# Optimization experiments

Measured on AMD Instinct MI355X. Metric: run time of the kernel, lower is better.

## Reference

```python
import jax, jax.numpy as jnp
import numpy as np

N, C, K2 = 40000, 128, 9  # active voxels, channels, 3x3 kernel taps
HEAD_OUT = {"hm": 3, "center": 2, "center_z": 1, "dim": 3, "rot": 2}
EPS = 1e-5
INIT_BIAS = -2.66


def setup_inputs() -> dict:
    key = jax.random.key(0)
    ks = jax.random.split(key, 16)
    feats = jax.random.normal(ks[0], (N, C), dtype=jnp.float32)
    # precomputed submanifold-conv neighbor indices (one per kernel tap, all valid)
    nbr_idx = jax.random.randint(ks[1], (N, K2), 0, N, dtype=jnp.int32)
    H = len(HEAD_OUT)
    inp = {"feats": feats, "nbr_idx": nbr_idx}
    # stacked 3x3 SubMConv weights for all heads (kaiming-ish scale)
    inp["W1"] = jax.random.normal(ks[2], (H, K2, C, C), dtype=jnp.float32) * (2.0 / (K2 * C)) ** 0.5
    inp["gamma"] = jnp.ones((H, C), jnp.float32)
    inp["beta"] = jnp.zeros((H, C), jnp.float32)
    for i, (name, oc) in enumerate(HEAD_OUT.items()):
        inp[f"w_{name}"] = jax.random.normal(ks[3 + i], (C, oc), dtype=jnp.float32) * (2.0 / C) ** 0.5
        inp[f"b_{name}"] = (jnp.full((oc,), INIT_BIAS, jnp.float32) if name == "hm"
                             else jnp.zeros((oc,), jnp.float32))
    return inp


def reference(feats, nbr_idx, W1, gamma, beta,
              w_hm, b_hm, w_center, b_center, w_center_z, b_center_z,
              w_dim, b_dim, w_rot, b_rot):
    # SubMConv2d as gather + contraction over kernel taps (shared by all heads)
    gathered = feats[nbr_idx]                       # [N, K2, C]
    y = jnp.einsum('nkc,hkcd->hnd', gathered, W1)   # [H, N, C]
    # BatchNorm1d (training-mode forward: biased batch stats over voxels) + ReLU
    mean = y.mean(axis=1, keepdims=True)
    var = y.var(axis=1, keepdims=True)
    y = jax.nn.relu((y - mean) * jax.lax.rsqrt(var + EPS) * gamma[:, None, :] + beta[:, None, :])
    # per-head 1x1 SubMConv with bias
    heads = [(w_hm, b_hm), (w_center, b_center), (w_center_z, b_center_z),
             (w_dim, b_dim), (w_rot, b_rot)]
    outs = [y[i] @ w + b for i, (w, b) in enumerate(heads)]
    # concat head outputs along channel: [N, 3+2+1+3+2] = [N, 11]
    return jnp.concatenate(outs, axis=-1)
```

## Files before the change

kernel.cpp:

```cpp
#include <hip/hip_runtime.h>
#include <stdint.h>

#define NVOX 40000
#define CCH  128
#define K2   9
#define NH   5
#define TILES 313

typedef __attribute__((ext_vector_type(8))) short bf16x8;
typedef __attribute__((ext_vector_type(4))) float f32x4;

__device__ __forceinline__ unsigned short f2b(float f) {
  union { float f; unsigned int u; } v; v.f = f;
  return (unsigned short)((v.u + 0x7fffu + ((v.u >> 16) & 1u)) >> 16);
}
__device__ __forceinline__ float b2f(unsigned short u) {
  union { unsigned int u; float f; } v; v.u = ((unsigned int)u) << 16;
  return v.f;
}
__device__ __forceinline__ void g2l16(const void* g, void* l) {
  __builtin_amdgcn_global_load_lds(
      (const __attribute__((address_space(1))) unsigned int*)g,
      (__attribute__((address_space(3))) unsigned int*)l, 16, 0, 0);
}
__device__ __forceinline__ int swz(int row, int col) {
  return row * 128 + ((((col >> 3) ^ (row & 15)) << 3) | (col & 7));
}

__global__ void prep(const float4* __restrict__ feats, ushort4* __restrict__ fb,
                     const float* __restrict__ w1, unsigned short* __restrict__ w1t,
                     float* __restrict__ sums) {
  __shared__ unsigned short t[64 * 34];
  int b = blockIdx.x;
  if (b < 5000) {
    int i = b * 256 + threadIdx.x;
    if (i < NVOX * CCH / 4) {
      float4 v = feats[i];
      ushort4 r;
      r.x = f2b(v.x); r.y = f2b(v.y); r.z = f2b(v.z); r.w = f2b(v.w);
      fb[i] = r;
    }
    return;
  }
  if (b == 5360) {
    for (int i = threadIdx.x; i < 2 * NH * CCH; i += 256) sums[i] = 0.f;
    return;
  }
  int bb = b - 5000;
  int tile = bb >> 3;
  int q = (bb >> 1) & 3;
  int dh = bb & 1;
  const float* src = w1 + (size_t)tile * 16384 + q * 32 * 128 + dh * 64;
  for (int e = threadIdx.x; e < 2048; e += 256) {
    int c = e >> 6, dd = e & 63;
    t[dd * 34 + c] = f2b(src[c * 128 + dd]);
  }
  __syncthreads();
  unsigned short* dst = w1t + (size_t)tile * 16384 + q * 32;
  for (int e = threadIdx.x; e < 2048; e += 256) {
    int d = e >> 5, c = e & 31;
    dst[(dh * 64 + d) * 128 + c] = t[d * 34 + c];
  }
}

__device__ __forceinline__ void stageBhalf8(unsigned short* dst, const unsigned short* wp_tap,
                                            int half, int wave, int lane) {
  int lrow = lane >> 3;
  int lch  = lane & 7;
#pragma unroll
  for (int i = 0; i < 2; ++i) {
    int blk = wave * 2 + i;
    g2l16(wp_tap + (blk * 8 + lrow) * 128 + half * 64 + ((lch ^ lrow) << 3),
          &dst[blk * 512]);
  }
}

__global__ void __launch_bounds__(512, 4) conv_gemm(
    const unsigned short* __restrict__ fb,
    const int* __restrict__ nbr,
    const unsigned short* __restrict__ w1t,
    unsigned short* __restrict__ yb,
    float* __restrict__ sums)
{
  __shared__ __align__(16) unsigned short Bsb[3][64 * 128];
  __shared__ int idxs[128 * K2];

  const int bid = blockIdx.x;
  const int s = bid / 40;
  const int r = bid % 40;
  const int h = r >> 3;
  const int x = r & 7;
  const int tile = s * 8 + x;
  if (tile >= TILES) return;
  const int n0 = tile * 128;

  const int tid = threadIdx.x;
  const int wave = tid >> 6;
  const int lane = tid & 63;
  const int m = lane & 15;
  const int quad = lane >> 4;
  const int wr = wave >> 1;
  const int wc = wave & 1;

  const unsigned short* wh = w1t + ((size_t)h * K2 << 14);

  for (int i = tid; i < 128 * K2; i += 512) {
    int rr = i / K2;
    int gn = n0 + rr; if (gn > NVOX - 1) gn = NVOX - 1;
    idxs[i] = nbr[gn * K2 + (i - rr * K2)];
  }
  __syncthreads();

  bf16x8 A[2][2][2];

  stageBhalf8(Bsb[0], wh, 0, wave, lane);
  {
    int i0 = idxs[(wr * 32 + m) * K2 + 0];
    int i1 = idxs[(wr * 32 + 16 + m) * K2 + 0];
    const unsigned short* p0 = fb + (size_t)i0 * CCH + quad * 8;
    const unsigned short* p1 = fb + (size_t)i1 * CCH + quad * 8;
    A[0][0][0] = *(const bf16x8*)(p0);
    A[0][0][1] = *(const bf16x8*)(p0 + 32);
    A[0][1][0] = *(const bf16x8*)(p1);
    A[0][1][1] = *(const bf16x8*)(p1 + 32);
  }
  stageBhalf8(Bsb[1], wh, 1, wave, lane);
  asm volatile("s_waitcnt vmcnt(2)" ::: "memory");
  __builtin_amdgcn_s_barrier();

  f32x4 acc[2][4] = {};

#pragma unroll
  for (int p = 0; p < 18; ++p) {
    const int par = p & 1;

    if (p < 17) {
      int tn = (p + 1) >> 1, kp = (p + 1) & 1;
      int i0 = idxs[(wr * 32 + m) * K2 + tn];
      int i1 = idxs[(wr * 32 + 16 + m) * K2 + tn];
      const unsigned short* p0 = fb + (size_t)i0 * CCH + kp * 64 + quad * 8;
      const unsigned short* p1 = fb + (size_t)i1 * CCH + kp * 64 + quad * 8;
      A[par ^ 1][0][0] = *(const bf16x8*)(p0);
      A[par ^ 1][0][1] = *(const bf16x8*)(p0 + 32);
      A[par ^ 1][1][0] = *(const bf16x8*)(p1);
      A[par ^ 1][1][1] = *(const bf16x8*)(p1 + 32);
    }
    if (p < 16)
      stageBhalf8(Bsb[(p + 2) % 3], wh + ((size_t)((p + 2) >> 1) << 14),
                  (p + 2) & 1, wave, lane);

    const unsigned short* Bcur = Bsb[p % 3];
#pragma unroll
    for (int kcL = 0; kcL < 2; ++kcL) {
      bf16x8 bfr[4];
#pragma unroll
      for (int nj = 0; nj < 4; ++nj) {
        int row = wc * 64 + nj * 16 + m;
        bfr[nj] = *(const bf16x8*)&Bcur[row * 64 + (((kcL * 4 + quad) ^ (m & 7)) << 3)];
      }
#pragma unroll
      for (int nj = 0; nj < 4; ++nj) {
        acc[0][nj] = __builtin_amdgcn_mfma_f32_16x16x32_bf16(A[par][0][kcL], bfr[nj], acc[0][nj], 0, 0, 0);
        acc[1][nj] = __builtin_amdgcn_mfma_f32_16x16x32_bf16(A[par][1][kcL], bfr[nj], acc[1][nj], 0, 0, 0);
      }
    }

    if (p < 16) {
      asm volatile("s_waitcnt vmcnt(2)" ::: "memory");
      __builtin_amdgcn_s_barrier();
    } else if (p == 16) {
      asm volatile("s_waitcnt vmcnt(0)" ::: "memory");
      __builtin_amdgcn_s_barrier();
    }
  }

  const bool full = (n0 + 128 <= NVOX);
  unsigned short* epi = &Bsb[0][0];

#pragma unroll
  for (int mi = 0; mi < 2; ++mi)
#pragma unroll
    for (int nj = 0; nj < 4; ++nj)
#pragma unroll
      for (int rr = 0; rr < 4; ++rr) {
        int row = wr * 32 + mi * 16 + quad * 4 + rr;
        int col = wc * 64 + nj * 16 + m;
        epi[swz(row, col)] = f2b(acc[mi][nj][rr]);
      }

  float psm[4], pq[4];
#pragma unroll
  for (int nj = 0; nj < 4; ++nj) {
    float sm = 0.f, q = 0.f;
#pragma unroll
    for (int mi = 0; mi < 2; ++mi)
#pragma unroll
      for (int rr = 0; rr < 4; ++rr) {
        float v = acc[mi][nj][rr];
        if (!full && n0 + wr * 32 + mi * 16 + quad * 4 + rr >= NVOX) v = 0.f;
        sm += v; q += v * v;
      }
    sm += __shfl_xor(sm, 16); q += __shfl_xor(q, 16);
    sm += __shfl_xor(sm, 32); q += __shfl_xor(q, 32);
    psm[nj] = sm; pq[nj] = q;
  }
  __syncthreads();

  float2* pb = (float2*)&Bsb[2][0];
  if (quad == 0)
#pragma unroll
    for (int nj = 0; nj < 4; ++nj)
      pb[(wc * 64 + nj * 16 + m) * 5 + wr] = make_float2(psm[nj], pq[nj]);

  for (int i = tid; i < 2048; i += 512) {
    int row = i >> 4;
    int c = i & 15;
    if (n0 + row < NVOX)
      *(bf16x8*)(yb + ((size_t)h * NVOX + n0 + row) * CCH + c * 8) =
          *(const bf16x8*)&epi[row * 128 + ((c ^ (row & 15)) << 3)];
  }
  __syncthreads();

  if (tid < 128) {
    float sm = 0.f, q = 0.f;
#pragma unroll
    for (int c = 0; c < 4; ++c) {
      float2 pv = pb[tid * 5 + c];
      sm += pv.x; q += pv.y;
    }
    atomicAdd(&sums[h * CCH + tid], sm);
    atomicAdd(&sums[NH * CCH + h * CCH + tid], q);
  }
}

__global__ void __launch_bounds__(256) head_fuse(
    const unsigned short* __restrict__ yb, const float* __restrict__ sums,
    const float* __restrict__ gamma, const float* __restrict__ beta,
    const float* __restrict__ w_hm, const float* __restrict__ b_hm,
    const float* __restrict__ w_ce, const float* __restrict__ b_ce,
    const float* __restrict__ w_cz, const float* __restrict__ b_cz,
    const float* __restrict__ w_dm, const float* __restrict__ b_dm,
    const float* __restrict__ w_rt, const float* __restrict__ b_rt,
    float* __restrict__ out)
{
  __shared__ unsigned short t[64 * 128];
  __shared__ float pbuf[4][64][3];
  __shared__ float scl[CCH], shf[CCH];

  const int tid = threadIdx.x;
  const int h  = blockIdx.x % NH;
  const int v0 = (blockIdx.x / NH) * 64;
  const int vx = tid & 63;
  const int qd = tid >> 6;

  const float* wp; const float* bp; int oc, off;
  switch (h) {
    case 0: wp = w_hm; bp = b_hm; oc = 3; off = 0; break;
    case 1: wp = w_ce; bp = b_ce; oc = 2; off = 3; break;
    case 2: wp = w_cz; bp = b_cz; oc = 1; off = 5; break;
    case 3: wp = w_dm; bp = b_dm; oc = 3; off = 6; break;
    default: wp = w_rt; bp = b_rt; oc = 2; off = 9; break;
  }

  if (tid < CCH) {
    int i = h * CCH + tid;
    float mean = sums[i] * (1.f / NVOX);
    float var = sums[NH * CCH + i] * (1.f / NVOX) - mean * mean;
    float rstd = rsqrtf(var + 1e-5f);
    float sc = rstd * gamma[i];
    scl[tid] = sc;
    shf[tid] = beta[i] - mean * sc;
  }
#pragma unroll
  for (int i = 0; i < 4; ++i) {
    int idx = i * 256 + tid;
    int row = idx >> 4, c = idx & 15;
    *(bf16x8*)&t[row * 128 + ((c ^ (row & 15)) << 3)] =
        *(const bf16x8*)(yb + ((size_t)h * NVOX + v0 + row) * CCH + c * 8);
  }
  __syncthreads();

  float p0 = 0.f, p1 = 0.f, p2 = 0.f;
#pragma unroll
  for (int qq = 0; qq < 4; ++qq) {
    int q8 = qd * 4 + qq;
    bf16x8 pk = *(const bf16x8*)&t[vx * 128 + ((q8 ^ (vx & 15)) << 3)];
#pragma unroll
    for (int e = 0; e < 8; ++e) {
      int d = q8 * 8 + e;
      float z = fmaf(b2f((unsigned short)pk[e]), scl[d], shf[d]);
      z = fmaxf(z, 0.f);
      const float* wr = wp + d * oc;
      p0 = fmaf(z, wr[0], p0);
      if (oc > 1) p1 = fmaf(z, wr[1], p1);
      if (oc > 2) p2 = fmaf(z, wr[2], p2);
    }
  }
  pbuf[qd][vx][0] = p0;
  if (oc > 1) pbuf[qd][vx][1] = p1;
  if (oc > 2) pbuf[qd][vx][2] = p2;
  __syncthreads();

  if (tid < 64) {
    float* op = out + (size_t)(v0 + tid) * 11 + off;
#pragma unroll
    for (int j = 0; j < 3; ++j)
      if (j < oc)
        op[j] = bp[j] + pbuf[0][tid][j] + pbuf[1][tid][j] + pbuf[2][tid][j] + pbuf[3][tid][j];
  }
}

extern "C" void kernel_launch(void* const* d_in, const int* in_sizes, int n_in,
                              void* d_out, int out_size, void* d_ws, size_t ws_size,
                              hipStream_t stream) {
  const float* feats = (const float*)d_in[0];
  const int*   nbr   = (const int*)d_in[1];
  const float* W1    = (const float*)d_in[2];
  const float* gamma = (const float*)d_in[3];
  const float* beta  = (const float*)d_in[4];
  const float* w_hm = (const float*)d_in[5];  const float* b_hm = (const float*)d_in[6];
  const float* w_ce = (const float*)d_in[7];  const float* b_ce = (const float*)d_in[8];
  const float* w_cz = (const float*)d_in[9];  const float* b_cz = (const float*)d_in[10];
  const float* w_dm = (const float*)d_in[11]; const float* b_dm = (const float*)d_in[12];
  const float* w_rt = (const float*)d_in[13]; const float* b_rt = (const float*)d_in[14];
  float* out = (float*)d_out;

  char* ws = (char*)d_ws;
  unsigned short* w1t = (unsigned short*)ws;
  unsigned short* fb  = (unsigned short*)(ws + 11796480);
  unsigned short* yb  = (unsigned short*)(ws + 22036480);
  float* sums = (float*)(ws + 73236480);

  prep<<<5361, 256, 0, stream>>>((const float4*)feats, (ushort4*)fb, W1, w1t, sums);
  conv_gemm<<<1600, 512, 0, stream>>>(fb, nbr, w1t, yb, sums);
  head_fuse<<<3125, 256, 0, stream>>>(yb, sums, gamma, beta, w_hm, b_hm, w_ce, b_ce,
                                      w_cz, b_cz, w_dm, b_dm, w_rt, b_rt, out);
}
```

Baseline: 270.8 us.

## Restructure conv GEMM to 32x32 MFMA with 4 waves and full-tap B staging

```diff
diff --git a/kernel.cpp b/kernel.cpp
--- a/kernel.cpp
+++ b/kernel.cpp
@@ -8,7 +8,7 @@
 #define TILES 313
 
 typedef __attribute__((ext_vector_type(8))) short bf16x8;
-typedef __attribute__((ext_vector_type(4))) float f32x4;
+typedef __attribute__((ext_vector_type(16))) float f32x16;
 
 __device__ __forceinline__ unsigned short f2b(float f) {
   union { float f; unsigned int u; } v; v.f = f;
@@ -63,26 +63,25 @@
   }
 }
 
-__device__ __forceinline__ void stageBhalf8(unsigned short* dst, const unsigned short* wp_tap,
-                                            int half, int wave, int lane) {
-  int lrow = lane >> 3;
-  int lch  = lane & 7;
-#pragma unroll
-  for (int i = 0; i < 2; ++i) {
-    int blk = wave * 2 + i;
-    g2l16(wp_tap + (blk * 8 + lrow) * 128 + half * 64 + ((lch ^ lrow) << 3),
-          &dst[blk * 512]);
-  }
-}
-
-__global__ void __launch_bounds__(512, 4) conv_gemm(
+__device__ __forceinline__ void stageB(unsigned short* dstbuf, const unsigned short* wp,
+                                       int wave, int lane) {
+  int lcol = lane & 15, lrow = lane >> 4;
+#pragma unroll
+  for (int i = 0; i < 8; ++i) {
+    int elem = wave * 4096 + i * 512;
+    int row = (elem >> 7) + lrow;
+    g2l16(wp + row * 128 + ((lcol ^ (row & 15)) << 3), &dstbuf[elem]);
+  }
+}
+
+__global__ void __launch_bounds__(256, 2) conv_gemm(
     const unsigned short* __restrict__ fb,
     const int* __restrict__ nbr,
     const unsigned short* __restrict__ w1t,
     unsigned short* __restrict__ yb,
     float* __restrict__ sums)
 {
-  __shared__ __align__(16) unsigned short Bsb[3][64 * 128];
+  __shared__ __align__(16) unsigned short Bsb[2][128 * 128];
   __shared__ int idxs[128 * K2];
 
   const int bid = blockIdx.x;
@@ -97,122 +96,106 @@
   const int tid = threadIdx.x;
   const int wave = tid >> 6;
   const int lane = tid & 63;
-  const int m = lane & 15;
-  const int quad = lane >> 4;
-  const int wr = wave >> 1;
-  const int wc = wave & 1;
+  const int l31 = lane & 31;
+  const int hi  = lane >> 5;
+  const int rg = wave >> 1;
+  const int cg = wave & 1;
 
   const unsigned short* wh = w1t + ((size_t)h * K2 << 14);
 
-  for (int i = tid; i < 128 * K2; i += 512) {
+  stageB(Bsb[0], wh, wave, lane);
+
+  for (int i = tid; i < 128 * K2; i += 256) {
     int rr = i / K2;
     int gn = n0 + rr; if (gn > NVOX - 1) gn = NVOX - 1;
     idxs[i] = nbr[gn * K2 + (i - rr * K2)];
   }
   __syncthreads();
 
-  bf16x8 A[2][2][2];
-
-  stageBhalf8(Bsb[0], wh, 0, wave, lane);
-  {
-    int i0 = idxs[(wr * 32 + m) * K2 + 0];
-    int i1 = idxs[(wr * 32 + 16 + m) * K2 + 0];
-    const unsigned short* p0 = fb + (size_t)i0 * CCH + quad * 8;
-    const unsigned short* p1 = fb + (size_t)i1 * CCH + quad * 8;
-    A[0][0][0] = *(const bf16x8*)(p0);
-    A[0][0][1] = *(const bf16x8*)(p0 + 32);
-    A[0][1][0] = *(const bf16x8*)(p1);
-    A[0][1][1] = *(const bf16x8*)(p1 + 32);
-  }
-  stageBhalf8(Bsb[1], wh, 1, wave, lane);
-  asm volatile("s_waitcnt vmcnt(2)" ::: "memory");
-  __builtin_amdgcn_s_barrier();
-
-  f32x4 acc[2][4] = {};
-
-#pragma unroll
-  for (int p = 0; p < 18; ++p) {
-    const int par = p & 1;
-
-    if (p < 17) {
-      int tn = (p + 1) >> 1, kp = (p + 1) & 1;
-      int i0 = idxs[(wr * 32 + m) * K2 + tn];
-      int i1 = idxs[(wr * 32 + 16 + m) * K2 + tn];
-      const unsigned short* p0 = fb + (size_t)i0 * CCH + kp * 64 + quad * 8;
-      const unsigned short* p1 = fb + (size_t)i1 * CCH + kp * 64 + quad * 8;
-      A[par ^ 1][0][0] = *(const bf16x8*)(p0);
-      A[par ^ 1][0][1] = *(const bf16x8*)(p0 + 32);
-      A[par ^ 1][1][0] = *(const bf16x8*)(p1);
-      A[par ^ 1][1][1] = *(const bf16x8*)(p1 + 32);
+  bf16x8 Ar[4][2];
+#define LOAD_A(SLOT, G)                                                        \
+  {                                                                            \
+    int tp = (G) >> 3, ksx = (G) & 7;                                          \
+    int i0 = idxs[(rg * 64 + l31) * K2 + tp];                                  \
+    int i1 = idxs[(rg * 64 + 32 + l31) * K2 + tp];                             \
+    Ar[SLOT][0] = *(const bf16x8*)(fb + (size_t)i0 * CCH + ksx * 16 + hi * 8); \
+    Ar[SLOT][1] = *(const bf16x8*)(fb + (size_t)i1 * CCH + ksx * 16 + hi * 8); \
+  }
+
+  LOAD_A(0, 0)
+  LOAD_A(1, 1)
+  LOAD_A(2, 2)
+  asm volatile("s_waitcnt vmcnt(0)" ::: "memory");
+  __syncthreads();
+
+  f32x16 acc[2][2] = {};
+
+#pragma unroll
+  for (int k = 0; k < K2; ++k) {
+    if (k + 1 < K2)
+      stageB(Bsb[(k + 1) & 1], wh + ((size_t)(k + 1) << 14), wave, lane);
+    const unsigned short* Bcur = Bsb[k & 1];
+
+#pragma unroll
+    for (int ks = 0; ks < 8; ++ks) {
+      const int g = k * 8 + ks;
+      if (g + 3 < 72) LOAD_A((g + 3) & 3, g + 3)
+      const int slotc = ((ks * 2 + hi) ^ (l31 & 15)) << 3;
+      bf16x8 b0 = *(const bf16x8*)&Bcur[(cg * 64 + l31) * 128 + slotc];
+      bf16x8 b1 = *(const bf16x8*)&Bcur[(cg * 64 + 32 + l31) * 128 + slotc];
+      acc[0][0] = __builtin_amdgcn_mfma_f32_32x32x16_bf16(Ar[g & 3][0], b0, acc[0][0], 0, 0, 0);
+      acc[0][1] = __builtin_amdgcn_mfma_f32_32x32x16_bf16(Ar[g & 3][0], b1, acc[0][1], 0, 0, 0);
+      acc[1][0] = __builtin_amdgcn_mfma_f32_32x32x16_bf16(Ar[g & 3][1], b0, acc[1][0], 0, 0, 0);
+      acc[1][1] = __builtin_amdgcn_mfma_f32_32x32x16_bf16(Ar[g & 3][1], b1, acc[1][1], 0, 0, 0);
     }
-    if (p < 16)
-      stageBhalf8(Bsb[(p + 2) % 3], wh + ((size_t)((p + 2) >> 1) << 14),
-                  (p + 2) & 1, wave, lane);
-
-    const unsigned short* Bcur = Bsb[p % 3];
-#pragma unroll
-    for (int kcL = 0; kcL < 2; ++kcL) {
-      bf16x8 bfr[4];
-#pragma unroll
-      for (int nj = 0; nj < 4; ++nj) {
-        int row = wc * 64 + nj * 16 + m;
-        bfr[nj] = *(const bf16x8*)&Bcur[row * 64 + (((kcL * 4 + quad) ^ (m & 7)) << 3)];
-      }
-#pragma unroll
-      for (int nj = 0; nj < 4; ++nj) {
-        acc[0][nj] = __builtin_amdgcn_mfma_f32_16x16x32_bf16(A[par][0][kcL], bfr[nj], acc[0][nj], 0, 0, 0);
-        acc[1][nj] = __builtin_amdgcn_mfma_f32_16x16x32_bf16(A[par][1][kcL], bfr[nj], acc[1][nj], 0, 0, 0);
-      }
-    }
-
-    if (p < 16) {
-      asm volatile("s_waitcnt vmcnt(2)" ::: "memory");
-      __builtin_amdgcn_s_barrier();
-    } else if (p == 16) {
-      asm volatile("s_waitcnt vmcnt(0)" ::: "memory");
+
+    if (k + 1 < K2) {
+      asm volatile("s_waitcnt vmcnt(6)" ::: "memory");
       __builtin_amdgcn_s_barrier();
     }
   }
+#undef LOAD_A
+  __syncthreads();
 
   const bool full = (n0 + 128 <= NVOX);
   unsigned short* epi = &Bsb[0][0];
-
-#pragma unroll
-  for (int mi = 0; mi < 2; ++mi)
-#pragma unroll
-    for (int nj = 0; nj < 4; ++nj)
-#pragma unroll
-      for (int rr = 0; rr < 4; ++rr) {
-        int row = wr * 32 + mi * 16 + quad * 4 + rr;
-        int col = wc * 64 + nj * 16 + m;
-        epi[swz(row, col)] = f2b(acc[mi][nj][rr]);
+#pragma unroll
+  for (int rt = 0; rt < 2; ++rt)
+#pragma unroll
+    for (int ct = 0; ct < 2; ++ct)
+#pragma unroll
+      for (int reg = 0; reg < 16; ++reg) {
+        int rloc = rg * 64 + rt * 32 + (reg & 3) + 8 * (reg >> 2) + 4 * hi;
+        int col = cg * 64 + ct * 32 + l31;
+        epi[swz(rloc, col)] = f2b(acc[rt][ct][reg]);
       }
 
-  float psm[4], pq[4];
-#pragma unroll
-  for (int nj = 0; nj < 4; ++nj) {
-    float sm = 0.f, q = 0.f;
-#pragma unroll
-    for (int mi = 0; mi < 2; ++mi)
-#pragma unroll
-      for (int rr = 0; rr < 4; ++rr) {
-        float v = acc[mi][nj][rr];
-        if (!full && n0 + wr * 32 + mi * 16 + quad * 4 + rr >= NVOX) v = 0.f;
-        sm += v; q += v * v;
+  float psm[2] = {0.f, 0.f}, pq[2] = {0.f, 0.f};
+#pragma unroll
+  for (int ct = 0; ct < 2; ++ct) {
+#pragma unroll
+    for (int rt = 0; rt < 2; ++rt)
+#pragma unroll
+      for (int reg = 0; reg < 16; ++reg) {
+        float v = acc[rt][ct][reg];
+        if (!full) {
+          int rloc = rg * 64 + rt * 32 + (reg & 3) + 8 * (reg >> 2) + 4 * hi;
+          if (n0 + rloc >= NVOX) v = 0.f;
+        }
+        psm[ct] += v; pq[ct] += v * v;
       }
-    sm += __shfl_xor(sm, 16); q += __shfl_xor(q, 16);
-    sm += __shfl_xor(sm, 32); q += __shfl_xor(q, 32);
-    psm[nj] = sm; pq[nj] = q;
-  }
-  __syncthreads();
-
-  float2* pb = (float2*)&Bsb[2][0];
-  if (quad == 0)
-#pragma unroll
-    for (int nj = 0; nj < 4; ++nj)
-      pb[(wc * 64 + nj * 16 + m) * 5 + wr] = make_float2(psm[nj], pq[nj]);
-
-  for (int i = tid; i < 2048; i += 512) {
+    psm[ct] += __shfl_xor(psm[ct], 32);
+    pq[ct]  += __shfl_xor(pq[ct], 32);
+  }
+  __syncthreads();
+
+  float2* pb = (float2*)&Bsb[1][0];
+  if (hi == 0)
+#pragma unroll
+    for (int ct = 0; ct < 2; ++ct)
+      pb[(cg * 64 + ct * 32 + l31) * 2 + rg] = make_float2(psm[ct], pq[ct]);
+
+  for (int i = tid; i < 2048; i += 256) {
     int row = i >> 4;
     int c = i & 15;
     if (n0 + row < NVOX)
@@ -222,14 +205,9 @@
   __syncthreads();
 
   if (tid < 128) {
-    float sm = 0.f, q = 0.f;
-#pragma unroll
-    for (int c = 0; c < 4; ++c) {
-      float2 pv = pb[tid * 5 + c];
-      sm += pv.x; q += pv.y;
-    }
-    atomicAdd(&sums[h * CCH + tid], sm);
-    atomicAdd(&sums[NH * CCH + h * CCH + tid], q);
+    float2 p0 = pb[tid * 2 + 0], p1 = pb[tid * 2 + 1];
+    atomicAdd(&sums[h * CCH + tid], p0.x + p1.x);
+    atomicAdd(&sums[NH * CCH + h * CCH + tid], p0.y + p1.y);
   }
 }
 
@@ -332,7 +310,7 @@
   float* sums = (float*)(ws + 73236480);
 
   prep<<<5361, 256, 0, stream>>>((const float4*)feats, (ushort4*)fb, W1, w1t, sums);
-  conv_gemm<<<1600, 512, 0, stream>>>(fb, nbr, w1t, yb, sums);
+  conv_gemm<<<1600, 256, 0, stream>>>(fb, nbr, w1t, yb, sums);
   head_fuse<<<3125, 256, 0, stream>>>(yb, sums, gamma, beta, w_hm, b_hm, w_ce, b_ce,
                                       w_cz, b_cz, w_dm, b_dm, w_rt, b_rt, out);
 }
```

After: 259.3 us. 4.2% less time.
